# Performance work log

Measured on AMD Instinct MI355X. Metric: run time of the kernel, lower is better.

## Reference

```python
import jax, jax.numpy as jnp
import numpy as np
from jax import lax

B, T, IN = 32, 512, 32
SNN, TS, HID, HOR = 128, 4, 128, 96
K = 3
THR = 1.0
EPS = 1e-5


def _spike(x):
    # heaviside: fires when (mem - threshold) > 0
    return (x > 0).astype(x.dtype)


def _lif_scan(xs, beta, thr):
    """snntorch Leaky (reset_mechanism='subtract'): mem_t = beta*mem_{t-1} + x_t - spk_{t-1}*thr; spk_t = H(mem_t - thr).
    xs: (S, B, C); beta: (C,). Returns spikes (S,B,C) and membrane (S,B,C)."""
    def step(carry, x):
        mem, rst = carry
        mem = beta * mem + x - rst * thr
        spk = _spike(mem - thr)
        return (mem, lax.stop_gradient(spk)), (spk, mem)
    z = jnp.zeros(xs.shape[1:], xs.dtype)
    _, (spks, mems) = lax.scan(step, (z, z), xs)
    return spks, mems


def setup_inputs() -> dict:
    key = jax.random.key(0)
    ks = jax.random.split(key, 10)
    def rn(k, shape, scale=0.05):
        return jax.random.normal(k, shape, dtype=jnp.float32) * scale
    return {
        "x": jax.random.normal(ks[0], (B, T, IN), dtype=jnp.float32),
        "conv_w": rn(ks[1], (SNN * TS, IN, K)),
        "conv_b": jnp.zeros((SNN * TS,), jnp.float32),
        "bn1_g": jnp.ones((SNN * TS,), jnp.float32),
        "bn1_b": jnp.zeros((SNN * TS,), jnp.float32),
        "beta1": jnp.full((SNN,), 0.9, jnp.float32),
        "bn2_g": jnp.ones((SNN,), jnp.float32),
        "bn2_b": jnp.zeros((SNN,), jnp.float32),
        "beta2": jnp.full((SNN,), 0.9, jnp.float32),
        "gru_wih": rn(ks[2], (3 * HID, IN + SNN)),
        "gru_whh": rn(ks[3], (3 * HID, HID)),
        "gru_bih": jnp.zeros((3 * HID,), jnp.float32),
        "gru_bhh": jnp.zeros((3 * HID,), jnp.float32),
        "q_w": rn(ks[4], (HID, HID)), "q_b": jnp.zeros((HID,), jnp.float32),
        "k_w": rn(ks[5], (HID, HID)), "k_b": jnp.zeros((HID,), jnp.float32),
        "v_w": rn(ks[6], (HID, HID)), "v_b": jnp.zeros((HID,), jnp.float32),
        "bn3_g": jnp.ones((HID,), jnp.float32),
        "bn3_b": jnp.zeros((HID,), jnp.float32),
        "head_w": rn(ks[7], (HOR, HID)),
        "head_b": jnp.zeros((HOR,), jnp.float32),
    }


def reference(x, conv_w, conv_b, bn1_g, bn1_b, beta1, bn2_g, bn2_b, beta2,
              gru_wih, gru_whh, gru_bih, gru_bhh, q_w, q_b, k_w, k_b, v_w, v_b,
              bn3_g, bn3_b, head_w, head_b):
    beta1 = jnp.clip(beta1, 0.0, 0.99)
    beta2 = jnp.clip(beta2, 0.0, 0.99)
    # --- ConvSpikeEncoder: Conv1d -> BatchNorm1d (training stats) -> LIF scan ---
    h = lax.conv_general_dilated(x.transpose(0, 2, 1), conv_w, (1,), [(K // 2, K // 2)],
                                 dimension_numbers=('NCH', 'OIH', 'NCH'))
    h = h + conv_b[None, :, None]  # (B, SNN*TS, T)
    m = h.mean((0, 2), keepdims=True)
    v = jnp.var(h, (0, 2), keepdims=True)
    h = (h - m) * lax.rsqrt(v + EPS) * bn1_g[None, :, None] + bn1_b[None, :, None]
    # (B, SNN*TS, T) -> (T*TS, B, SNN), step index = t*TS + s
    h = h.transpose(0, 2, 1).reshape(B, T * TS, SNN).transpose(1, 0, 2)
    spk_enc, _ = _lif_scan(h, beta1, THR)  # (T*TS, B, SNN)
    # --- per-step BatchNorm1d over batch dim, then second LIF ---
    m2 = spk_enc.mean(1, keepdims=True)
    v2 = jnp.var(spk_enc, 1, keepdims=True)
    h2 = (spk_enc - m2) * lax.rsqrt(v2 + EPS) * bn2_g + bn2_b
    _, mem_rec = _lif_scan(h2, beta2, THR)  # (T*TS, B, SNN)
    # --- downsample membrane: mean over TS sub-steps ---
    mem_down = mem_rec.transpose(1, 0, 2).reshape(B, T, TS, SNN).mean(2)  # (B, T, SNN)
    hc = jnp.concatenate([x, mem_down], -1)  # (B, T, IN+SNN)
    # --- GRU (PyTorch gate order r,z,n) ---
    def gstep(hprev, xt):
        gi = xt @ gru_wih.T + gru_bih
        gh = hprev @ gru_whh.T + gru_bhh
        ir, iz, inn = jnp.split(gi, 3, -1)
        hr, hz, hn = jnp.split(gh, 3, -1)
        r = jax.nn.sigmoid(ir + hr)
        zg = jax.nn.sigmoid(iz + hz)
        n = jnp.tanh(inn + r * hn)
        hnew = (1.0 - zg) * n + zg * hprev
        return hnew, hnew
    _, gru_seq = lax.scan(gstep, jnp.zeros((B, HID), x.dtype), hc.transpose(1, 0, 2))
    g = gru_seq.transpose(1, 0, 2)  # (B, T, HID)
    # --- SpikingAttention: sigmoid(QK^T*scale) @ V, mean over T, BatchNorm ---
    Q = g @ q_w.T + q_b
    Kk = g @ k_w.T + k_b
    V = g @ v_w.T + v_b
    attn = jax.nn.sigmoid(jnp.einsum('btc,bsc->bts', Q, Kk) * (HID ** -0.5))
    out = jnp.einsum('bts,bsc->btc', attn, V).mean(1)  # (B, HID)
    m3 = out.mean(0, keepdims=True)
    v3 = jnp.var(out, 0, keepdims=True)
    out = (out - m3) * lax.rsqrt(v3 + EPS) * bn3_g + bn3_b
    return out @ head_w.T + head_b  # (B, HOR)
```

## Files before the change

### kernel.cpp

```cpp
#include <hip/hip_runtime.h>
#include <math.h>

#define EPSV 1e-5f

#if __has_builtin(__builtin_amdgcn_exp2f)
#define EXP2F(x) __builtin_amdgcn_exp2f(x)
#else
#define EXP2F(x) exp2f(x)
#endif
#if __has_builtin(__builtin_amdgcn_rcpf)
#define RCPF(x) __builtin_amdgcn_rcpf(x)
#else
#define RCPF(x) (1.0f/(x))
#endif

__device__ __forceinline__ float fsigmoid(float x){
  return RCPF(1.0f + EXP2F(-1.4426950408889634f * x));
}
__device__ __forceinline__ float ftanh(float x){
  return RCPF(0.5f + 0.5f * EXP2F(-2.8853900817779268f * x)) - 1.0f;
}
__device__ __forceinline__ unsigned short f2bf(float f){
  unsigned u = __float_as_uint(f);
  return (unsigned short)((u + 0x7FFFu + ((u >> 16) & 1u)) >> 16);
}

typedef __attribute__((ext_vector_type(8))) short bf16x8;
typedef __attribute__((ext_vector_type(4))) float f32x4;
typedef __attribute__((ext_vector_type(2))) _Float16 f16x2;
typedef __attribute__((ext_vector_type(8))) _Float16 f16x8;

#if __has_builtin(__builtin_amdgcn_fdot2)
#define FDOT2(a,b,c) __builtin_amdgcn_fdot2(a,b,c,false)
#else
__device__ __forceinline__ float FDOT2(f16x2 a, f16x2 b, float c){
  return c + (float)a[0]*(float)b[0] + (float)a[1]*(float)b[1];
}
#endif

__device__ __forceinline__ float dot8(f16x8 w, f16x8 h, float acc){
  f16x2 w0 = {w[0],w[1]}, w1 = {w[2],w[3]}, w2 = {w[4],w[5]}, w3 = {w[6],w[7]};
  f16x2 h0 = {h[0],h[1]}, h1 = {h[2],h[3]}, h2 = {h[4],h[5]}, h3 = {h[6],h[7]};
  acc = FDOT2(w0,h0,acc); acc = FDOT2(w1,h1,acc);
  acc = FDOT2(w2,h2,acc); acc = FDOT2(w3,h3,acc);
  return acc;
}

__global__ __launch_bounds__(256) void k_conv(const float* __restrict__ x, const float* __restrict__ w,
        const float* __restrict__ cb, float* __restrict__ hp, float* __restrict__ s1g, float* __restrict__ s2g,
        unsigned short* __restrict__ x_bf){
  __shared__ float xs[32*321];
  __shared__ float ws[32*97];
  __shared__ float bs[32];
  const int tid = threadIdx.x;
  const int t0 = blockIdx.x * 8;
  const int n0 = blockIdx.y * 8;
  for (int idx = tid; idx < 32*10*32; idx += 256){
    int bq = idx / 320; int rem = idx - bq*320; int tt = rem >> 5; int i = rem & 31;
    int tg = t0 - 1 + tt;
    float v = 0.f;
    if (tg >= 0 && tg < 512) v = x[(bq*512 + tg)*32 + i];
    xs[bq*321 + tt*32 + i] = v;
  }
  for (int idx = tid; idx < 32*96; idx += 256){
    int row = idx / 96; int within = idx - row*96;
    int ss = row >> 3; int nl = row & 7;
    int c = ss*128 + n0 + nl;
    ws[row*97 + within] = w[c*96 + within];
  }
  if (tid < 32){
    int ss = tid >> 3, nl = tid & 7;
    bs[tid] = cb[ss*128 + n0 + nl];
  }
  __syncthreads();
  if (blockIdx.y == 0){
    for (int idx = tid; idx < 32*8*32; idx += 256){
      int bq = idx >> 8; int rem = idx & 255; int tt = rem >> 5; int i = rem & 31;
      x_bf[(bq*512 + t0 + tt)*32 + i] = f2bf(xs[bq*321 + (tt+1)*32 + i]);
    }
  }
  const int b = tid & 31;
  const int nl = tid >> 5;
  float acc[4][8];
  #pragma unroll
  for (int ss = 0; ss < 4; ++ss){
    float bv = bs[ss*8 + nl];
    #pragma unroll
    for (int t = 0; t < 8; ++t) acc[ss][t] = bv;
  }
  for (int i = 0; i < 32; ++i){
    #pragma unroll
    for (int k = 0; k < 3; ++k){
      float w0 = ws[(0*8+nl)*97 + i*3 + k];
      float w1 = ws[(1*8+nl)*97 + i*3 + k];
      float w2 = ws[(2*8+nl)*97 + i*3 + k];
      float w3 = ws[(3*8+nl)*97 + i*3 + k];
      #pragma unroll
      for (int t = 0; t < 8; ++t){
        float xv = xs[b*321 + (t+k)*32 + i];
        acc[0][t] += xv*w0; acc[1][t] += xv*w1; acc[2][t] += xv*w2; acc[3][t] += xv*w3;
      }
    }
  }
  #pragma unroll
  for (int ss = 0; ss < 4; ++ss){
    int n = n0 + nl;
    float s1 = 0.f, s2 = 0.f;
    #pragma unroll
    for (int t = 0; t < 8; ++t){
      float v = acc[ss][t];
      int s = (t0 + t)*4 + ss;
      hp[s*4096 + n*32 + b] = v;
      s1 += v; s2 += v*v;
    }
    #pragma unroll
    for (int off = 1; off < 32; off <<= 1){
      s1 += __shfl_xor(s1, off);
      s2 += __shfl_xor(s2, off);
    }
    if (b == 0){
      int c = ss*128 + n;
      atomicAdd(&s1g[c], s1);
      atomicAdd(&s2g[c], s2);
    }
  }
}

__global__ void k_bn1(const float* __restrict__ s1g, const float* __restrict__ s2g,
                      const float* __restrict__ g, const float* __restrict__ bb,
                      float* __restrict__ a1, float* __restrict__ b1){
  int c = threadIdx.x;
  float m = s1g[c] * (1.f/16384.f);
  float v = s2g[c] * (1.f/16384.f) - m*m;
  float sc = g[c] * rsqrtf(v + EPSV);
  a1[c] = sc;
  b1[c] = bb[c] - m*sc;
}

__global__ __launch_bounds__(256) void k_cvt_all(const float* __restrict__ wih,
        const float* __restrict__ qw, const float* __restrict__ kw, const float* __restrict__ vw,
        const float* __restrict__ whh,
        unsigned short* __restrict__ wih_bf, unsigned short* __restrict__ wqkv_bf,
        _Float16* __restrict__ whh_h){
  int i = blockIdx.x*256 + threadIdx.x;
  if (i < 61440){ wih_bf[i] = f2bf(wih[i]); return; }
  int r = i - 61440;
  if (r < 16384){ wqkv_bf[r] = f2bf(qw[r]); return; }
  r -= 16384;
  if (r < 16384){ wqkv_bf[16384 + r] = f2bf(kw[r]); return; }
  r -= 16384;
  if (r < 16384){ wqkv_bf[32768 + r] = f2bf(vw[r]); return; }
  r -= 16384;
  if (r < 49152){ whh_h[r] = (_Float16)whh[r]; }
}

__global__ __launch_bounds__(256) void k_lif(const float* __restrict__ hp,
        const float* __restrict__ a1, const float* __restrict__ b1,
        const float* __restrict__ beta1, const float* __restrict__ g2v, const float* __restrict__ b2v,
        const float* __restrict__ beta2, unsigned short* __restrict__ md_bf){
  const int tid = threadIdx.x;
  const int b = tid & 31;
  const int n = blockIdx.x * 8 + (tid >> 5);
  float a1r0 = a1[0*128+n], a1r1 = a1[1*128+n], a1r2 = a1[2*128+n], a1r3 = a1[3*128+n];
  float b1r0 = b1[0*128+n], b1r1 = b1[1*128+n], b1r2 = b1[2*128+n], b1r3 = b1[3*128+n];
  float be1 = fminf(fmaxf(beta1[n], 0.f), 0.99f);
  float be2 = fminf(fmaxf(beta2[n], 0.f), 0.99f);
  float g2 = g2v[n], bb2 = b2v[n];
  float m1 = 0.f, r1 = 0.f, m2 = 0.f, r2 = 0.f;
  const float* base = hp + n*32 + b;
  float c0 = base[0], c1 = base[4096], c2 = base[2*4096], c3 = base[3*4096];

#define LIF_STEP(CV, A1R, B1R) { \
    float x1 = CV*A1R + B1R; \
    m1 = be1*m1 + x1 - r1; \
    bool sp = (m1 > 1.0f); \
    unsigned long long mk = __ballot(sp); \
    float spk = sp ? 1.f : 0.f; r1 = spk; \
    unsigned hf = (tid & 32) ? (unsigned)(mk >> 32) : (unsigned)mk; \
    float mean = (float)__popc(hf) * 0.03125f; \
    float var = mean - mean*mean; \
    float h2 = (spk - mean) * rsqrtf(var + EPSV) * g2 + bb2; \
    m2 = be2*m2 + h2 - r2; \
    r2 = (m2 > 1.0f) ? 1.f : 0.f; \
    accd += m2; }

  for (int t = 0; t < 512; ++t){
    float n0v = 0.f, n1v = 0.f, n2v = 0.f, n3v = 0.f;
    if (t < 511){
      const float* nb = base + (size_t)(t+1)*16384;
      n0v = nb[0]; n1v = nb[4096]; n2v = nb[2*4096]; n3v = nb[3*4096];
    }
    float accd = 0.f;
    LIF_STEP(c0, a1r0, b1r0)
    LIF_STEP(c1, a1r1, b1r1)
    LIF_STEP(c2, a1r2, b1r2)
    LIF_STEP(c3, a1r3, b1r3)
    md_bf[(b*512 + t)*128 + n] = f2bf(accd * 0.25f);
    c0 = n0v; c1 = n1v; c2 = n2v; c3 = n3v;
  }
#undef LIF_STEP
}

__global__ __launch_bounds__(256) void k_mm_gi(const unsigned short* __restrict__ xbf,
        const unsigned short* __restrict__ mdbf, const unsigned short* __restrict__ wihbf,
        const float* __restrict__ bih, float* __restrict__ gi2){
  const int tid = threadIdx.x;
  const int w = tid >> 6, l = tid & 63;
  const int c16 = l & 15, kg = l >> 4;
  const int m0 = (blockIdx.x*4 + w) * 16;
  const int mrow = m0 + c16;
  bf16x8 a0 = *(const bf16x8*)&xbf[(size_t)mrow*32 + kg*8];
  const unsigned short* mdp = &mdbf[(size_t)mrow*128 + kg*8];
  bf16x8 a1 = *(const bf16x8*)(mdp + 0);
  bf16x8 a2 = *(const bf16x8*)(mdp + 32);
  bf16x8 a3 = *(const bf16x8*)(mdp + 64);
  bf16x8 a4 = *(const bf16x8*)(mdp + 96);
  for (int nt = 0; nt < 24; ++nt){
    int n0 = nt*16;
    const unsigned short* wp = &wihbf[(size_t)(n0 + c16)*160 + kg*8];
    bf16x8 b0 = *(const bf16x8*)(wp + 0);
    bf16x8 b1 = *(const bf16x8*)(wp + 32);
    bf16x8 b2 = *(const bf16x8*)(wp + 64);
    bf16x8 b3 = *(const bf16x8*)(wp + 96);
    bf16x8 b4 = *(const bf16x8*)(wp + 128);
    f32x4 acc = {0.f,0.f,0.f,0.f};
    acc = __builtin_amdgcn_mfma_f32_16x16x32_bf16(a0, b0, acc, 0, 0, 0);
    acc = __builtin_amdgcn_mfma_f32_16x16x32_bf16(a1, b1, acc, 0, 0, 0);
    acc = __builtin_amdgcn_mfma_f32_16x16x32_bf16(a2, b2, acc, 0, 0, 0);
    acc = __builtin_amdgcn_mfma_f32_16x16x32_bf16(a3, b3, acc, 0, 0, 0);
    acc = __builtin_amdgcn_mfma_f32_16x16x32_bf16(a4, b4, acc, 0, 0, 0);
    int n = n0 + c16;
    int gate = n >> 7;
    int jj = n & 127;
    float bias = bih[n];
    #pragma unroll
    for (int r = 0; r < 4; ++r){
      gi2[(size_t)(m0 + kg*4 + r)*512 + jj*4 + gate] = acc[r] + bias;
    }
  }
}

template<int SEL>
__device__ __forceinline__ float dpp_qp(float x){
  return __int_as_float(__builtin_amdgcn_mov_dpp(__float_as_int(x), SEL, 0xF, 0xF, true));
}
__device__ __forceinline__ float qbc(float x, int u){
  switch(u){
    case 0: return dpp_qp<0x00>(x);
    case 1: return dpp_qp<0x55>(x);
    case 2: return dpp_qp<0xAA>(x);
    default: return dpp_qp<0xFF>(x);
  }
}
__global__ __launch_bounds__(512, 2) void k_gru(const float* __restrict__ gi2, const _Float16* __restrict__ whh_h,
        const float* __restrict__ bhh, unsigned short* __restrict__ gout_bf){
  const int b = blockIdx.x;
  const int tid = threadIdx.x;
  const int j = tid >> 2;
  const int q = tid & 3;
  __shared__ _Float16 hs[2][144];
  const _Float16* wbr = whh_h + (size_t)(      j)*128 + q*32;
  const _Float16* wbz = whh_h + (size_t)(128 + j)*128 + q*32;
  const _Float16* wbn = whh_h + (size_t)(256 + j)*128 + q*32;
  f16x8 wr0 = *(const f16x8*)(wbr+ 0), wr1 = *(const f16x8*)(wbr+ 8),
        wr2 = *(const f16x8*)(wbr+16), wr3 = *(const f16x8*)(wbr+24);
  f16x8 wz0 = *(const f16x8*)(wbz+ 0), wz1 = *(const f16x8*)(wbz+ 8),
        wz2 = *(const f16x8*)(wbz+16), wz3 = *(const f16x8*)(wbz+24);
  f16x8 wn0 = *(const f16x8*)(wbn+ 0), wn1 = *(const f16x8*)(wbn+ 8),
        wn2 = *(const f16x8*)(wbn+16), wn3 = *(const f16x8*)(wbn+24);
  float bh_r = 0.f, bh_z = 0.f, bh_n = 0.f;
  if (!q){
    bh_r = bhh[j]; bh_z = bhh[128+j]; bh_n = bhh[256+j];
  }
  const float* gib = gi2 + (size_t)b*512*512;
  f32x4 G = *(const f32x4*)(gib + (size_t)q*512 + j*4);
  if (tid < 128) hs[0][tid] = (_Float16)0.f;
  float hprev = 0.f;
  __syncthreads();
  for (int g = 0; g < 128; ++g){
    f32x4 N = {0.f,0.f,0.f,0.f};
    if (g < 127) N = *(const f32x4*)(gib + (size_t)(4*(g+1) + q)*512 + j*4);
    #pragma unroll
    for (int u = 0; u < 4; ++u){
      const int t = g*4 + u;
      float gr = qbc(G[0], u);
      float gz = qbc(G[1], u);
      float gn = qbc(G[2], u);
      const f16x8* hq = (const f16x8*)&hs[t & 1][q*32];
      f16x8 h0 = hq[0], h1 = hq[1], h2 = hq[2], h3 = hq[3];
      float ar = 0.f, az = 0.f, an = 0.f;
      ar = dot8(wr0,h0,ar); ar = dot8(wr1,h1,ar); ar = dot8(wr2,h2,ar); ar = dot8(wr3,h3,ar);
      az = dot8(wz0,h0,az); az = dot8(wz1,h1,az); az = dot8(wz2,h2,az); az = dot8(wz3,h3,az);
      an = dot8(wn0,h0,an); an = dot8(wn1,h1,an); an = dot8(wn2,h2,an); an = dot8(wn3,h3,an);
      ar += dpp_qp<0xB1>(ar); ar += dpp_qp<0x4E>(ar);
      az += dpp_qp<0xB1>(az); az += dpp_qp<0x4E>(az);
      an += dpp_qp<0xB1>(an); an += dpp_qp<0x4E>(an);
      if (!q){
        float r = fsigmoid(gr + ar + bh_r);
        float z = fsigmoid(gz + az + bh_z);
        float nn = ftanh(gn + r*(an + bh_n));
        float hn = (1.f - z)*nn + z*hprev;
        hprev = hn;
        hs[(t + 1) & 1][j] = (_Float16)hn;
        gout_bf[((size_t)b*512 + t)*128 + j] = f2bf(hn);
      }
      __syncthreads();
    }
    G = N;
  }
}

__global__ __launch_bounds__(256) void k_mm_qkv(const unsigned short* __restrict__ gbf,
        const unsigned short* __restrict__ wbf, const float* __restrict__ qb2,
        const float* __restrict__ kb2, const float* __restrict__ vb2,
        unsigned short* __restrict__ Qbf, unsigned short* __restrict__ Kbf, float* __restrict__ Vb){
  const int tid = threadIdx.x;
  const int w = tid >> 6, l = tid & 63;
  const int c16 = l & 15, kg = l >> 4;
  const int m0 = (blockIdx.x*4 + w) * 16;
  const unsigned short* gp = &gbf[(size_t)(m0 + c16)*128 + kg*8];
  bf16x8 a0 = *(const bf16x8*)(gp + 0);
  bf16x8 a1 = *(const bf16x8*)(gp + 32);
  bf16x8 a2 = *(const bf16x8*)(gp + 64);
  bf16x8 a3 = *(const bf16x8*)(gp + 96);
  for (int nt = 0; nt < 24; ++nt){
    int n0 = nt*16;
    const unsigned short* wp = &wbf[(size_t)(n0 + c16)*128 + kg*8];
    bf16x8 b0 = *(const bf16x8*)(wp + 0);
    bf16x8 b1 = *(const bf16x8*)(wp + 32);
    bf16x8 b2 = *(const bf16x8*)(wp + 64);
    bf16x8 b3 = *(const bf16x8*)(wp + 96);
    f32x4 acc = {0.f,0.f,0.f,0.f};
    acc = __builtin_amdgcn_mfma_f32_16x16x32_bf16(a0, b0, acc, 0, 0, 0);
    acc = __builtin_amdgcn_mfma_f32_16x16x32_bf16(a1, b1, acc, 0, 0, 0);
    acc = __builtin_amdgcn_mfma_f32_16x16x32_bf16(a2, b2, acc, 0, 0, 0);
    acc = __builtin_amdgcn_mfma_f32_16x16x32_bf16(a3, b3, acc, 0, 0, 0);
    int n = n0 + c16;
    if (n < 128){
      float bias = qb2[n];
      #pragma unroll
      for (int r = 0; r < 4; ++r)
        Qbf[(size_t)(m0 + kg*4 + r)*128 + n] = f2bf(acc[r] + bias);
    } else if (n < 256){
      float bias = kb2[n-128];
      #pragma unroll
      for (int r = 0; r < 4; ++r)
        Kbf[(size_t)(m0 + kg*4 + r)*128 + (n-128)] = f2bf(acc[r] + bias);
    } else {
      float bias = vb2[n-256];
      #pragma unroll
      for (int r = 0; r < 4; ++r)
        Vb[(size_t)(m0 + kg*4 + r)*128 + (n-256)] = acc[r] + bias;
    }
  }
}

__global__ __launch_bounds__(256) void k_attn(const unsigned short* __restrict__ Qbf,
        const unsigned short* __restrict__ Kbf, float* __restrict__ av){
  const int tid = threadIdx.x;
  const int b  = blockIdx.x;
  const int st = blockIdx.y;
  const int w  = tid >> 6;
  const int l  = tid & 63;
  const int c16 = l & 15;
  const int kg  = l >> 4;
  const float SC = 0.08838834764831845f;
  const unsigned short* kp = Kbf + ((size_t)(b*512 + st*64 + w*16 + c16))*128 + kg*8;
  bf16x8 a0 = *(const bf16x8*)(kp + 0);
  bf16x8 a1 = *(const bf16x8*)(kp + 32);
  bf16x8 a2 = *(const bf16x8*)(kp + 64);
  bf16x8 a3 = *(const bf16x8*)(kp + 96);
  const unsigned short* qb = Qbf + ((size_t)(b*512 + c16))*128 + kg*8;
  float ps0 = 0.f, ps1 = 0.f, ps2 = 0.f, ps3 = 0.f;
  for (int tt = 0; tt < 32; ++tt){
    const unsigned short* qp = qb + (size_t)tt*16*128;
    bf16x8 b0 = *(const bf16x8*)(qp + 0);
    bf16x8 b1 = *(const bf16x8*)(qp + 32);
    bf16x8 b2 = *(const bf16x8*)(qp + 64);
    bf16x8 b3 = *(const bf16x8*)(qp + 96);
    f32x4 acc = {0.f, 0.f, 0.f, 0.f};
    acc = __builtin_amdgcn_mfma_f32_16x16x32_bf16(a0, b0, acc, 0, 0, 0);
    acc = __builtin_amdgcn_mfma_f32_16x16x32_bf16(a1, b1, acc, 0, 0, 0);
    acc = __builtin_amdgcn_mfma_f32_16x16x32_bf16(a2, b2, acc, 0, 0, 0);
    acc = __builtin_amdgcn_mfma_f32_16x16x32_bf16(a3, b3, acc, 0, 0, 0);
    ps0 += fsigmoid(acc[0]*SC);
    ps1 += fsigmoid(acc[1]*SC);
    ps2 += fsigmoid(acc[2]*SC);
    ps3 += fsigmoid(acc[3]*SC);
  }
  #pragma unroll
  for (int off = 1; off < 16; off <<= 1){
    ps0 += __shfl_xor(ps0, off);
    ps1 += __shfl_xor(ps1, off);
    ps2 += __shfl_xor(ps2, off);
    ps3 += __shfl_xor(ps3, off);
  }
  if (c16 == 0){
    int sb = st*64 + w*16 + kg*4;
    av[b*512 + sb + 0] = ps0 * (1.f/512.f);
    av[b*512 + sb + 1] = ps1 * (1.f/512.f);
    av[b*512 + sb + 2] = ps2 * (1.f/512.f);
    av[b*512 + sb + 3] = ps3 * (1.f/512.f);
  }
}

__global__ __launch_bounds__(128) void k_av(const float* __restrict__ av, const float* __restrict__ Vb,
        float* __restrict__ out0){
  int b = blockIdx.x, c = threadIdx.x;
  float a0 = 0.f, a1 = 0.f, a2 = 0.f, a3 = 0.f;
  for (int s = 0; s < 512; s += 4){
    a0 += av[b*512 + s+0] * Vb[(size_t)(b*512 + s+0)*128 + c];
    a1 += av[b*512 + s+1] * Vb[(size_t)(b*512 + s+1)*128 + c];
    a2 += av[b*512 + s+2] * Vb[(size_t)(b*512 + s+2)*128 + c];
    a3 += av[b*512 + s+3] * Vb[(size_t)(b*512 + s+3)*128 + c];
  }
  out0[b*128 + c] = (a0 + a1) + (a2 + a3);
}

__global__ __launch_bounds__(256) void k_final(const float* __restrict__ out0,
        const float* __restrict__ g3, const float* __restrict__ b3,
        const float* __restrict__ hw, const float* __restrict__ hb, float* __restrict__ out){
  __shared__ float on[32*132];
  const int tid = threadIdx.x;
  if (tid < 128){
    int c = tid;
    float s = 0.f;
    for (int bq = 0; bq < 32; ++bq) s += out0[bq*128 + c];
    float m = s * (1.f/32.f);
    float v = 0.f;
    for (int bq = 0; bq < 32; ++bq){ float d = out0[bq*128 + c] - m; v += d*d; }
    v *= (1.f/32.f);
    float sc = g3[c] * rsqrtf(v + EPSV);
    float sh = b3[c] - m*sc;
    for (int bq = 0; bq < 32; ++bq) on[bq*132 + c] = out0[bq*128 + c]*sc + sh;
  }
  __syncthreads();
  for (int o = tid; o < 32*96; o += 256){
    int bq = o / 96, hh = o - bq*96;
    float acc = hb[hh];
    for (int k = 0; k < 128; ++k) acc += on[bq*132 + k] * hw[hh*128 + k];
    out[o] = acc;
  }
}

extern "C" void kernel_launch(void* const* d_in, const int* in_sizes, int n_in,
                              void* d_out, int out_size, void* d_ws, size_t ws_size,
                              hipStream_t stream){
  const float* x      = (const float*)d_in[0];
  const float* conv_w = (const float*)d_in[1];
  const float* conv_b = (const float*)d_in[2];
  const float* bn1_g  = (const float*)d_in[3];
  const float* bn1_b  = (const float*)d_in[4];
  const float* beta1  = (const float*)d_in[5];
  const float* bn2_g  = (const float*)d_in[6];
  const float* bn2_b  = (const float*)d_in[7];
  const float* beta2  = (const float*)d_in[8];
  const float* g_wih  = (const float*)d_in[9];
  const float* g_whh  = (const float*)d_in[10];
  const float* g_bih  = (const float*)d_in[11];
  const float* g_bhh  = (const float*)d_in[12];
  const float* q_w    = (const float*)d_in[13];
  const float* q_b    = (const float*)d_in[14];
  const float* k_w    = (const float*)d_in[15];
  const float* k_b    = (const float*)d_in[16];
  const float* v_w    = (const float*)d_in[17];
  const float* v_b    = (const float*)d_in[18];
  const float* bn3_g  = (const float*)d_in[19];
  const float* bn3_b  = (const float*)d_in[20];
  const float* head_w = (const float*)d_in[21];
  const float* head_b = (const float*)d_in[22];

  char* ws = (char*)d_ws;
  float* hp            = (float*)ws;
  unsigned short* md_bf= (unsigned short*)(ws + 33554432);
  unsigned short* g_bf = (unsigned short*)(ws + 37748736);
  unsigned short* x_bf = (unsigned short*)(ws + 41943040);
  unsigned short* wih_bf  = (unsigned short*)(ws + 42991616);
  unsigned short* wqkv_bf = (unsigned short*)(ws + 43114496);
  _Float16* whh_h      = (_Float16*)(ws + 43212800);
  float* s1g = (float*)(ws + 50331648);
  float* s2g = (float*)(ws + 50331648 + 2048);
  float* a1  = (float*)(ws + 50331648 + 4096);
  float* b1  = (float*)(ws + 50331648 + 6144);
  float* av  = (float*)(ws + 50331648 + 8192);
  float* out0= (float*)(ws + 50331648 + 8192 + 65536);
  float* gi2 = (float*)ws;
  unsigned short* Qbf = (unsigned short*)ws;
  unsigned short* Kbf = (unsigned short*)(ws + 4194304);
  float* Vb  = (float*)(ws + 8388608);

  (void)hipMemsetAsync(ws + 50331648, 0, 4096, stream);

  k_conv<<<dim3(64, 16), 256, 0, stream>>>(x, conv_w, conv_b, hp, s1g, s2g, x_bf);
  k_bn1<<<1, 512, 0, stream>>>(s1g, s2g, bn1_g, bn1_b, a1, b1);
  k_cvt_all<<<624, 256, 0, stream>>>(g_wih, q_w, k_w, v_w, g_whh, wih_bf, wqkv_bf, whh_h);
  k_lif<<<16, 256, 0, stream>>>(hp, a1, b1, beta1, bn2_g, bn2_b, beta2, md_bf);
  k_mm_gi<<<256, 256, 0, stream>>>(x_bf, md_bf, wih_bf, g_bih, gi2);
  k_gru<<<32, 512, 0, stream>>>(gi2, whh_h, g_bhh, g_bf);
  k_mm_qkv<<<256, 256, 0, stream>>>(g_bf, wqkv_bf, q_b, k_b, v_b, Qbf, Kbf, Vb);
  k_attn<<<dim3(32, 8), 256, 0, stream>>>(Qbf, Kbf, av);
  k_av<<<32, 128, 0, stream>>>(av, Vb, out0);
  k_final<<<1, 256, 0, stream>>>(out0, bn3_g, bn3_b, head_w, head_b, (float*)d_out);
}
```

Before: 665.4 us.

## Compute GRU recurrent matmul with bf16 MFMA, four batches per block

The GRU recurrence is rewritten so each block handles four batch rows and computes the hidden-to-hidden product with bf16 MFMA instructions, where it previously used f16 dot2 instructions per hidden unit. The recurrent weights are converted to bf16 and held in registers, and gate results pass through shared memory before the elementwise update. This removes the per-step packed-dot and DPP reduction chain, but leaves only 8 blocks, wastes MFMA rows (4 of 16 used), adds two barriers per step, and lowers hidden-state precision from f16 to bf16.

New measurement: 850.2 us. 27.8% more time.

```diff
diff --git a/kernel.cpp b/kernel.cpp
--- a/kernel.cpp
+++ b/kernel.cpp
@@ -27,24 +27,6 @@
 
 typedef __attribute__((ext_vector_type(8))) short bf16x8;
 typedef __attribute__((ext_vector_type(4))) float f32x4;
-typedef __attribute__((ext_vector_type(2))) _Float16 f16x2;
-typedef __attribute__((ext_vector_type(8))) _Float16 f16x8;
-
-#if __has_builtin(__builtin_amdgcn_fdot2)
-#define FDOT2(a,b,c) __builtin_amdgcn_fdot2(a,b,c,false)
-#else
-__device__ __forceinline__ float FDOT2(f16x2 a, f16x2 b, float c){
-  return c + (float)a[0]*(float)b[0] + (float)a[1]*(float)b[1];
-}
-#endif
-
-__device__ __forceinline__ float dot8(f16x8 w, f16x8 h, float acc){
-  f16x2 w0 = {w[0],w[1]}, w1 = {w[2],w[3]}, w2 = {w[4],w[5]}, w3 = {w[6],w[7]};
-  f16x2 h0 = {h[0],h[1]}, h1 = {h[2],h[3]}, h2 = {h[4],h[5]}, h3 = {h[6],h[7]};
-  acc = FDOT2(w0,h0,acc); acc = FDOT2(w1,h1,acc);
-  acc = FDOT2(w2,h2,acc); acc = FDOT2(w3,h3,acc);
-  return acc;
-}
 
 __global__ __launch_bounds__(256) void k_conv(const float* __restrict__ x, const float* __restrict__ w,
         const float* __restrict__ cb, float* __restrict__ hp, float* __restrict__ s1g, float* __restrict__ s2g,
@@ -141,7 +123,7 @@
         const float* __restrict__ qw, const float* __restrict__ kw, const float* __restrict__ vw,
         const float* __restrict__ whh,
         unsigned short* __restrict__ wih_bf, unsigned short* __restrict__ wqkv_bf,
-        _Float16* __restrict__ whh_h){
+        unsigned short* __restrict__ whh_bf){
   int i = blockIdx.x*256 + threadIdx.x;
   if (i < 61440){ wih_bf[i] = f2bf(wih[i]); return; }
   int r = i - 61440;
@@ -151,7 +133,7 @@
   r -= 16384;
   if (r < 16384){ wqkv_bf[32768 + r] = f2bf(vw[r]); return; }
   r -= 16384;
-  if (r < 49152){ whh_h[r] = (_Float16)whh[r]; }
+  if (r < 49152){ whh_bf[r] = f2bf(whh[r]); }
 }
 
 __global__ __launch_bounds__(256) void k_lif(const float* __restrict__ hp,
@@ -240,73 +222,70 @@
   }
 }
 
-template<int SEL>
-__device__ __forceinline__ float dpp_qp(float x){
-  return __int_as_float(__builtin_amdgcn_mov_dpp(__float_as_int(x), SEL, 0xF, 0xF, true));
-}
-__device__ __forceinline__ float qbc(float x, int u){
-  switch(u){
-    case 0: return dpp_qp<0x00>(x);
-    case 1: return dpp_qp<0x55>(x);
-    case 2: return dpp_qp<0xAA>(x);
-    default: return dpp_qp<0xFF>(x);
-  }
-}
-__global__ __launch_bounds__(512, 2) void k_gru(const float* __restrict__ gi2, const _Float16* __restrict__ whh_h,
-        const float* __restrict__ bhh, unsigned short* __restrict__ gout_bf){
-  const int b = blockIdx.x;
-  const int tid = threadIdx.x;
-  const int j = tid >> 2;
-  const int q = tid & 3;
-  __shared__ _Float16 hs[2][144];
-  const _Float16* wbr = whh_h + (size_t)(      j)*128 + q*32;
-  const _Float16* wbz = whh_h + (size_t)(128 + j)*128 + q*32;
-  const _Float16* wbn = whh_h + (size_t)(256 + j)*128 + q*32;
-  f16x8 wr0 = *(const f16x8*)(wbr+ 0), wr1 = *(const f16x8*)(wbr+ 8),
-        wr2 = *(const f16x8*)(wbr+16), wr3 = *(const f16x8*)(wbr+24);
-  f16x8 wz0 = *(const f16x8*)(wbz+ 0), wz1 = *(const f16x8*)(wbz+ 8),
-        wz2 = *(const f16x8*)(wbz+16), wz3 = *(const f16x8*)(wbz+24);
-  f16x8 wn0 = *(const f16x8*)(wbn+ 0), wn1 = *(const f16x8*)(wbn+ 8),
-        wn2 = *(const f16x8*)(wbn+16), wn3 = *(const f16x8*)(wbn+24);
-  float bh_r = 0.f, bh_z = 0.f, bh_n = 0.f;
-  if (!q){
-    bh_r = bhh[j]; bh_z = bhh[128+j]; bh_n = bhh[256+j];
-  }
-  const float* gib = gi2 + (size_t)b*512*512;
-  f32x4 G = *(const f32x4*)(gib + (size_t)q*512 + j*4);
-  if (tid < 128) hs[0][tid] = (_Float16)0.f;
+__global__ __launch_bounds__(512, 2) void k_gru(const float* __restrict__ gi2,
+        const unsigned short* __restrict__ whh_bf, const float* __restrict__ bhh,
+        unsigned short* __restrict__ gout_bf){
+  __shared__ unsigned short hsm[16][136];
+  __shared__ float gates[4][396];
+  const int tid = threadIdx.x;
+  const int wv  = tid >> 6;
+  const int l   = tid & 63;
+  const int c16 = l & 15;
+  const int kg  = l >> 4;
+  bf16x8 Bf0[4], Bf1[4], Bf2[4];
+  #pragma unroll
+  for (int c = 0; c < 4; ++c){
+    Bf0[c] = *(const bf16x8*)&whh_bf[(size_t)(wv*48 +  0 + c16)*128 + c*32 + kg*8];
+    Bf1[c] = *(const bf16x8*)&whh_bf[(size_t)(wv*48 + 16 + c16)*128 + c*32 + kg*8];
+    Bf2[c] = *(const bf16x8*)&whh_bf[(size_t)(wv*48 + 32 + c16)*128 + c*32 + kg*8];
+  }
+  const int b  = tid >> 7;
+  const int j  = tid & 127;
+  const int bg = blockIdx.x*4 + b;
+  const float bh_r = bhh[j], bh_z = bhh[128+j], bh_n = bhh[256+j];
+  const float* gib = gi2 + (size_t)bg*512*512 + j*4;
   float hprev = 0.f;
+  for (int i2 = tid; i2 < 16*136; i2 += 512) ((unsigned short*)hsm)[i2] = 0;
   __syncthreads();
-  for (int g = 0; g < 128; ++g){
-    f32x4 N = {0.f,0.f,0.f,0.f};
-    if (g < 127) N = *(const f32x4*)(gib + (size_t)(4*(g+1) + q)*512 + j*4);
-    #pragma unroll
-    for (int u = 0; u < 4; ++u){
-      const int t = g*4 + u;
-      float gr = qbc(G[0], u);
-      float gz = qbc(G[1], u);
-      float gn = qbc(G[2], u);
-      const f16x8* hq = (const f16x8*)&hs[t & 1][q*32];
-      f16x8 h0 = hq[0], h1 = hq[1], h2 = hq[2], h3 = hq[3];
-      float ar = 0.f, az = 0.f, an = 0.f;
-      ar = dot8(wr0,h0,ar); ar = dot8(wr1,h1,ar); ar = dot8(wr2,h2,ar); ar = dot8(wr3,h3,ar);
-      az = dot8(wz0,h0,az); az = dot8(wz1,h1,az); az = dot8(wz2,h2,az); az = dot8(wz3,h3,az);
-      an = dot8(wn0,h0,an); an = dot8(wn1,h1,an); an = dot8(wn2,h2,an); an = dot8(wn3,h3,an);
-      ar += dpp_qp<0xB1>(ar); ar += dpp_qp<0x4E>(ar);
-      az += dpp_qp<0xB1>(az); az += dpp_qp<0x4E>(az);
-      an += dpp_qp<0xB1>(an); an += dpp_qp<0x4E>(an);
-      if (!q){
-        float r = fsigmoid(gr + ar + bh_r);
-        float z = fsigmoid(gz + az + bh_z);
-        float nn = ftanh(gn + r*(an + bh_n));
-        float hn = (1.f - z)*nn + z*hprev;
-        hprev = hn;
-        hs[(t + 1) & 1][j] = (_Float16)hn;
-        gout_bf[((size_t)b*512 + t)*128 + j] = f2bf(hn);
+  f32x4 G0 = *(const f32x4*)(gib);
+  f32x4 G1 = *(const f32x4*)(gib + 512);
+  for (int t = 0; t < 512; ++t){
+    bf16x8 A0 = *(const bf16x8*)&hsm[c16][kg*8 +  0];
+    bf16x8 A1 = *(const bf16x8*)&hsm[c16][kg*8 + 32];
+    bf16x8 A2 = *(const bf16x8*)&hsm[c16][kg*8 + 64];
+    bf16x8 A3 = *(const bf16x8*)&hsm[c16][kg*8 + 96];
+    f32x4 a0 = {0.f,0.f,0.f,0.f}, a1 = {0.f,0.f,0.f,0.f}, a2 = {0.f,0.f,0.f,0.f};
+    a0 = __builtin_amdgcn_mfma_f32_16x16x32_bf16(A0, Bf0[0], a0, 0,0,0);
+    a0 = __builtin_amdgcn_mfma_f32_16x16x32_bf16(A1, Bf0[1], a0, 0,0,0);
+    a0 = __builtin_amdgcn_mfma_f32_16x16x32_bf16(A2, Bf0[2], a0, 0,0,0);
+    a0 = __builtin_amdgcn_mfma_f32_16x16x32_bf16(A3, Bf0[3], a0, 0,0,0);
+    a1 = __builtin_amdgcn_mfma_f32_16x16x32_bf16(A0, Bf1[0], a1, 0,0,0);
+    a1 = __builtin_amdgcn_mfma_f32_16x16x32_bf16(A1, Bf1[1], a1, 0,0,0);
+    a1 = __builtin_amdgcn_mfma_f32_16x16x32_bf16(A2, Bf1[2], a1, 0,0,0);
+    a1 = __builtin_amdgcn_mfma_f32_16x16x32_bf16(A3, Bf1[3], a1, 0,0,0);
+    a2 = __builtin_amdgcn_mfma_f32_16x16x32_bf16(A0, Bf2[0], a2, 0,0,0);
+    a2 = __builtin_amdgcn_mfma_f32_16x16x32_bf16(A1, Bf2[1], a2, 0,0,0);
+    a2 = __builtin_amdgcn_mfma_f32_16x16x32_bf16(A2, Bf2[2], a2, 0,0,0);
+    a2 = __builtin_amdgcn_mfma_f32_16x16x32_bf16(A3, Bf2[3], a2, 0,0,0);
+    if (kg == 0){
+      #pragma unroll
+      for (int r = 0; r < 4; ++r){
+        gates[r][wv*48 +  0 + c16] = a0[r];
+        gates[r][wv*48 + 16 + c16] = a1[r];
+        gates[r][wv*48 + 32 + c16] = a2[r];
       }
-      __syncthreads();
-    }
-    G = N;
+    }
+    __syncthreads();
+    float rr = fsigmoid(G0[0] + gates[b][j]       + bh_r);
+    float zz = fsigmoid(G0[1] + gates[b][128 + j] + bh_z);
+    float nn = ftanh   (G0[2] + rr*(gates[b][256 + j] + bh_n));
+    float hn = (1.f - zz)*nn + zz*hprev;
+    hprev = hn;
+    hsm[b][j] = f2bf(hn);
+    gout_bf[((size_t)bg*512 + t)*128 + j] = f2bf(hn);
+    G0 = G1;
+    if (t < 510) G1 = *(const f32x4*)(gib + (size_t)(t+2)*512);
+    __syncthreads();
   }
 }
 
@@ -477,7 +456,7 @@
   unsigned short* x_bf = (unsigned short*)(ws + 41943040);
   unsigned short* wih_bf  = (unsigned short*)(ws + 42991616);
   unsigned short* wqkv_bf = (unsigned short*)(ws + 43114496);
-  _Float16* whh_h      = (_Float16*)(ws + 43212800);
+  unsigned short* whh_bf  = (unsigned short*)(ws + 43212800);
   float* s1g = (float*)(ws + 50331648);
   float* s2g = (float*)(ws + 50331648 + 2048);
   float* a1  = (float*)(ws + 50331648 + 4096);
@@ -493,10 +472,10 @@
 
   k_conv<<<dim3(64, 16), 256, 0, stream>>>(x, conv_w, conv_b, hp, s1g, s2g, x_bf);
   k_bn1<<<1, 512, 0, stream>>>(s1g, s2g, bn1_g, bn1_b, a1, b1);
-  k_cvt_all<<<624, 256, 0, stream>>>(g_wih, q_w, k_w, v_w, g_whh, wih_bf, wqkv_bf, whh_h);
+  k_cvt_all<<<624, 256, 0, stream>>>(g_wih, q_w, k_w, v_w, g_whh, wih_bf, wqkv_bf, whh_bf);
   k_lif<<<16, 256, 0, stream>>>(hp, a1, b1, beta1, bn2_g, bn2_b, beta2, md_bf);
   k_mm_gi<<<256, 256, 0, stream>>>(x_bf, md_bf, wih_bf, g_bih, gi2);
-  k_gru<<<32, 512, 0, stream>>>(gi2, whh_h, g_bhh, g_bf);
+  k_gru<<<8, 512, 0, stream>>>(gi2, whh_bf, g_bhh, g_bf);
   k_mm_qkv<<<256, 256, 0, stream>>>(g_bf, wqkv_bf, q_b, k_b, v_b, Qbf, Kbf, Vb);
   k_attn<<<dim3(32, 8), 256, 0, stream>>>(Qbf, Kbf, av);
   k_av<<<32, 128, 0, stream>>>(av, Vb, out0);
```

## Coalesce LIF output stores via transposed buffer and deepen input prefetch

Applied to the files above, without the earlier changes.

The LIF kernel now writes its bf16 membrane-mean output in a (t, n, b) layout, so each warp's stores are contiguous across the batch lanes instead of strided by 128. A new small transpose kernel then uses LDS to convert that buffer back to the (b, t, n) layout that the GEMM expects. Input prefetch in the serial LIF loop is also deepened from one step ahead to two. The cost is an extra kernel launch plus an extra read and write pass over a 4 MB buffer. The temporary buffer shares its workspace region with g_bf, which is safe only because g_bf is written later.

New measurement: 635.0 us. 4.6% less time.

```diff
diff --git a/kernel.cpp b/kernel.cpp
--- a/kernel.cpp
+++ b/kernel.cpp
@@ -26,6 +26,7 @@
 }
 
 typedef __attribute__((ext_vector_type(8))) short bf16x8;
+typedef __attribute__((ext_vector_type(8))) short s16x8;
 typedef __attribute__((ext_vector_type(4))) float f32x4;
 typedef __attribute__((ext_vector_type(2))) _Float16 f16x2;
 typedef __attribute__((ext_vector_type(8))) _Float16 f16x8;
@@ -157,7 +158,7 @@
 __global__ __launch_bounds__(256) void k_lif(const float* __restrict__ hp,
         const float* __restrict__ a1, const float* __restrict__ b1,
         const float* __restrict__ beta1, const float* __restrict__ g2v, const float* __restrict__ b2v,
-        const float* __restrict__ beta2, unsigned short* __restrict__ md_bf){
+        const float* __restrict__ beta2, unsigned short* __restrict__ md_t){
   const int tid = threadIdx.x;
   const int b = tid & 31;
   const int n = blockIdx.x * 8 + (tid >> 5);
@@ -169,6 +170,8 @@
   float m1 = 0.f, r1 = 0.f, m2 = 0.f, r2 = 0.f;
   const float* base = hp + n*32 + b;
   float c0 = base[0], c1 = base[4096], c2 = base[2*4096], c3 = base[3*4096];
+  const float* nb1 = base + 16384;
+  float d0 = nb1[0], d1 = nb1[4096], d2 = nb1[2*4096], d3 = nb1[3*4096];
 
 #define LIF_STEP(CV, A1R, B1R) { \
     float x1 = CV*A1R + B1R; \
@@ -185,20 +188,45 @@
     accd += m2; }
 
   for (int t = 0; t < 512; ++t){
-    float n0v = 0.f, n1v = 0.f, n2v = 0.f, n3v = 0.f;
-    if (t < 511){
-      const float* nb = base + (size_t)(t+1)*16384;
-      n0v = nb[0]; n1v = nb[4096]; n2v = nb[2*4096]; n3v = nb[3*4096];
+    float e0 = 0.f, e1 = 0.f, e2 = 0.f, e3 = 0.f;
+    if (t < 510){
+      const float* nb = base + (size_t)(t+2)*16384;
+      e0 = nb[0]; e1 = nb[4096]; e2 = nb[2*4096]; e3 = nb[3*4096];
     }
     float accd = 0.f;
     LIF_STEP(c0, a1r0, b1r0)
     LIF_STEP(c1, a1r1, b1r1)
     LIF_STEP(c2, a1r2, b1r2)
     LIF_STEP(c3, a1r3, b1r3)
-    md_bf[(b*512 + t)*128 + n] = f2bf(accd * 0.25f);
-    c0 = n0v; c1 = n1v; c2 = n2v; c3 = n3v;
+    md_t[((t*128) + n)*32 + b] = f2bf(accd * 0.25f);
+    c0 = d0; c1 = d1; c2 = d2; c3 = d3;
+    d0 = e0; d1 = e1; d2 = e2; d3 = e3;
   }
 #undef LIF_STEP
+}
+
+__global__ __launch_bounds__(256) void k_tr(const unsigned short* __restrict__ md_t,
+        unsigned short* __restrict__ md_bf){
+  __shared__ unsigned short l[128][40];
+  const int t = blockIdx.x;
+  const int tid = threadIdx.x;
+  const unsigned short* src = md_t + (size_t)t*4096;
+  #pragma unroll
+  for (int r = 0; r < 2; ++r){
+    int idx = tid*16 + r*8;
+    s16x8 v = *(const s16x8*)(src + idx);
+    int nn = idx >> 5, b0 = idx & 31;
+    #pragma unroll
+    for (int e = 0; e < 8; ++e) l[nn][b0 + e] = (unsigned short)v[e];
+  }
+  __syncthreads();
+  const int b = tid >> 3, seg = tid & 7;
+  unsigned short tmp[16];
+  #pragma unroll
+  for (int i = 0; i < 16; ++i) tmp[i] = l[seg*16 + i][b];
+  unsigned short* dst = md_bf + (size_t)(b*512 + t)*128 + seg*16;
+  *(s16x8*)(dst + 0) = *(s16x8*)&tmp[0];
+  *(s16x8*)(dst + 8) = *(s16x8*)&tmp[8];
 }
 
 __global__ __launch_bounds__(256) void k_mm_gi(const unsigned short* __restrict__ xbf,
@@ -473,6 +501,7 @@
   char* ws = (char*)d_ws;
   float* hp            = (float*)ws;
   unsigned short* md_bf= (unsigned short*)(ws + 33554432);
+  unsigned short* md_t = (unsigned short*)(ws + 37748736);
   unsigned short* g_bf = (unsigned short*)(ws + 37748736);
   unsigned short* x_bf = (unsigned short*)(ws + 41943040);
   unsigned short* wih_bf  = (unsigned short*)(ws + 42991616);
@@ -494,7 +523,8 @@
   k_conv<<<dim3(64, 16), 256, 0, stream>>>(x, conv_w, conv_b, hp, s1g, s2g, x_bf);
   k_bn1<<<1, 512, 0, stream>>>(s1g, s2g, bn1_g, bn1_b, a1, b1);
   k_cvt_all<<<624, 256, 0, stream>>>(g_wih, q_w, k_w, v_w, g_whh, wih_bf, wqkv_bf, whh_h);
-  k_lif<<<16, 256, 0, stream>>>(hp, a1, b1, beta1, bn2_g, bn2_b, beta2, md_bf);
+  k_lif<<<16, 256, 0, stream>>>(hp, a1, b1, beta1, bn2_g, bn2_b, beta2, md_t);
+  k_tr<<<512, 256, 0, stream>>>(md_t, md_bf);
   k_mm_gi<<<256, 256, 0, stream>>>(x_bf, md_bf, wih_bf, g_bih, gi2);
   k_gru<<<32, 512, 0, stream>>>(gi2, whh_h, g_bhh, g_bf);
   k_mm_qkv<<<256, 256, 0, stream>>>(g_bf, wqkv_bf, q_b, k_b, v_b, Qbf, Kbf, Vb);
```
